# Performance work log

Hardware: AMD Instinct MI355X
Metric: run time of the kernel (lower is better)

## Reference

```python
import jax, jax.numpy as jnp
import numpy as np

NUM_HEADS = 8


def setup_inputs() -> dict:
    key = jax.random.key(0)
    ks = jax.random.split(key, 7)
    B, Tq, Tkv, J, C = 16, 243, 243, 17, 256
    q = jax.random.normal(ks[0], (B, Tq, J, C), dtype=jnp.float32)
    kv = jax.random.normal(ks[1], (B, Tkv, J, C), dtype=jnp.float32)
    s = 1.0 / np.sqrt(C)
    Wq = jax.random.normal(ks[2], (C, C), dtype=jnp.float32) * s
    Wk = jax.random.normal(ks[3], (C, C), dtype=jnp.float32) * s
    Wv = jax.random.normal(ks[4], (C, C), dtype=jnp.float32) * s
    Wp = jax.random.normal(ks[5], (C, C), dtype=jnp.float32) * s
    bp = jnp.zeros((C,), dtype=jnp.float32)
    return {"q": q, "kv": kv, "Wq": Wq, "Wk": Wk, "Wv": Wv, "Wp": Wp, "bp": bp}


def reference(q, kv, Wq, Wk, Wv, Wp, bp):
    # q: [B, Tq, J, C], kv: [B, Tkv, J, C]
    b, tq, j, d = q.shape
    t_kv = kv.shape[1]
    h = NUM_HEADS
    hd = d // h
    scale = hd ** (-0.5)

    def split_heads(x, t):
        # [B, T, J, C] -> [B, H, J, T, hd]  (matches permute(0,3,2,1,4))
        return x.reshape(b, t, j, h, hd).transpose(0, 3, 2, 1, 4)

    q_p = split_heads(q @ Wq.T, tq)
    k_p = split_heads(kv @ Wk.T, t_kv)
    v_p = split_heads(kv @ Wv.T, t_kv)

    # attn: [B, H, J, Tq, Tkv]
    attn = jnp.einsum('bhjqe,bhjke->bhjqk', q_p, k_p) * scale
    attn = jax.nn.softmax(attn, axis=-1)
    # out: [B, H, J, Tq, hd] -> [B, Tq, J, C]
    out = jnp.einsum('bhjqk,bhjke->bhjqe', attn, v_p)
    out = out.transpose(0, 3, 2, 1, 4).reshape(b, tq, j, d)
    out = out @ Wp.T + bp
    return (attn, out)
```

## Files before the change

kernel.cpp:

```cpp
#include <hip/hip_runtime.h>

typedef _Float16 f16;
typedef _Float16 f16x8 __attribute__((ext_vector_type(8)));
typedef _Float16 f16x4 __attribute__((ext_vector_type(4)));
typedef float f32x4 __attribute__((ext_vector_type(4)));
typedef float f32x4a __attribute__((ext_vector_type(4), aligned(4)));

#define B_DIM 16
#define T_DIM 243
#define J_DIM 17
#define C_DIM 256
#define H_DIM 8
#define HD_DIM 32
#define M_DIM (B_DIM * T_DIM * J_DIM)
#define NSLICE (B_DIM * H_DIM * J_DIM)
#define TJ (T_DIM * J_DIM)

#define QP_OFF 0ull
#define KP_OFF ((unsigned long long)NSLICE * T_DIM * HD_DIM)
#define VPT_OFF (2ull * KP_OFF)
#define O_OFF (VPT_OFF + (unsigned long long)NSLICE * HD_DIM * 256)
#define WF_OFF (O_OFF + (unsigned long long)M_DIM * C_DIM)
#define ATTN_SZ ((unsigned long long)NSLICE * T_DIM * T_DIM)

#define SWZ(row, col) ((col) ^ (((row) & 7) << 3))

__global__ __launch_bounds__(256)
void wconv_kernel(const float* __restrict__ Wq, const float* __restrict__ Wk,
                  const float* __restrict__ Wv, const float* __restrict__ Wp,
                  f16* __restrict__ wf)
{
    int i = blockIdx.x * 256 + threadIdx.x;
    const float* src = (i < 65536) ? Wq : (i < 131072) ? Wk : (i < 196608) ? Wv : Wp;
    wf[i] = (f16)src[i & 65535];
}

__global__ __launch_bounds__(256)
void proj_kernel(const float* __restrict__ q, const float* __restrict__ kv,
                 const f16* __restrict__ wf, f16* __restrict__ ws)
{
    const int which = blockIdx.z;
    const float* A = (which == 0) ? q : kv;
    const f16* W = wf + which * 65536;
    f16* out = ws + (which == 0 ? QP_OFF : KP_OFF);

    const int tid = threadIdx.x;
    const int w = tid >> 6, l = tid & 63;
    const int lm = l & 15, g = l >> 4;
    const int m0 = blockIdx.x * 64;

    int arow = m0 + w * 16 + lm;
    const bool mok = arow < M_DIM;
    if (!mok) arow = M_DIM - 1;
    const float* Ab = A + (size_t)arow * C_DIM + g * 8;

    f16x8 af[8];
#pragma unroll
    for (int kk = 0; kk < 8; ++kk) {
        f32x4 a0 = *(const f32x4*)(Ab + kk * 32);
        f32x4 a1 = *(const f32x4*)(Ab + kk * 32 + 4);
#pragma unroll
        for (int j = 0; j < 4; ++j) { af[kk][j] = (f16)a0[j]; af[kk][4 + j] = (f16)a1[j]; }
    }

    f32x4 acc[16] = {};
#pragma unroll
    for (int nt = 0; nt < 16; ++nt) {
        const f16* Wb = W + (size_t)(nt * 16 + lm) * C_DIM + g * 8;
#pragma unroll
        for (int kk = 0; kk < 8; ++kk) {
            f16x8 bf = *(const f16x8*)(Wb + kk * 32);
            acc[nt] = __builtin_amdgcn_mfma_f32_16x16x32_f16(bf, af[kk], acc[nt], 0, 0, 0);
        }
    }

    int b = arow / TJ;
    int rem = arow - b * TJ;
    int t = rem / J_DIM;
    int jj = rem - t * J_DIM;
    if (mok) {
#pragma unroll
        for (int nt = 0; nt < 16; ++nt) {
            int n0 = nt * 16 + g * 4;
            int h = n0 >> 5, e = n0 & 31;
            int sI = (b * H_DIM + h) * J_DIM + jj;
            f16x4 v;
#pragma unroll
            for (int r = 0; r < 4; ++r) v[r] = (f16)acc[nt][r];
            *(f16x4*)(out + (size_t)sI * (T_DIM * HD_DIM) + (size_t)t * HD_DIM + e) = v;
        }
    }
}

__global__ __launch_bounds__(256)
void vproj_kernel(const float* __restrict__ kv, const f16* __restrict__ wv,
                  f16* __restrict__ vpt)
{
    __shared__ f16 Sv[64 * 72];

    const int bj = blockIdx.z;
    const int b = bj / J_DIM, j = bj - b * J_DIM;
    const int t0 = blockIdx.x * 64;
    const int n0 = blockIdx.y * 64;

    const int tid = threadIdx.x;
    const int w = tid >> 6, l = tid & 63;
    const int lm = l & 15, g = l >> 4;

    int t = t0 + w * 16 + lm;
    if (t > T_DIM - 1) t = T_DIM - 1;
    const float* Ab = kv + ((size_t)b * TJ + (size_t)t * J_DIM + j) * C_DIM + g * 8;

    f16x8 af[8];
#pragma unroll
    for (int kk = 0; kk < 8; ++kk) {
        f32x4 a0 = *(const f32x4*)(Ab + kk * 32);
        f32x4 a1 = *(const f32x4*)(Ab + kk * 32 + 4);
#pragma unroll
        for (int jj = 0; jj < 4; ++jj) { af[kk][jj] = (f16)a0[jj]; af[kk][4 + jj] = (f16)a1[jj]; }
    }

    f32x4 acc[4] = {};
#pragma unroll
    for (int nt = 0; nt < 4; ++nt) {
        const f16* Wb = wv + (size_t)(n0 + nt * 16 + lm) * C_DIM + g * 8;
#pragma unroll
        for (int kk = 0; kk < 8; ++kk) {
            f16x8 bf = *(const f16x8*)(Wb + kk * 32);
            acc[nt] = __builtin_amdgcn_mfma_f32_16x16x32_f16(af[kk], bf, acc[nt], 0, 0, 0);
        }
    }

    const int trow = w * 16 + g * 4;
#pragma unroll
    for (int nt = 0; nt < 4; ++nt) {
        int nl = nt * 16 + lm;
#pragma unroll
        for (int r = 0; r < 4; ++r)
            Sv[nl * 72 + trow + r] = (f16)acc[nt][r];
    }
    __syncthreads();

    const int nl = tid >> 2, tp = tid & 3;
    const int n = n0 + nl;
    const int h = n >> 5, e = n & 31;
    const int s = (b * H_DIM + h) * J_DIM + j;
    const int tbase = t0 + tp * 16;

    f16x8 v0 = *(const f16x8*)&Sv[nl * 72 + tp * 16];
    f16x8 v1 = *(const f16x8*)&Sv[nl * 72 + tp * 16 + 8];
    if (tbase + 15 > T_DIM - 1) {
#pragma unroll
        for (int i = 0; i < 8; ++i) {
            if (tbase + i > T_DIM - 1) v0[i] = (f16)0;
            if (tbase + 8 + i > T_DIM - 1) v1[i] = (f16)0;
        }
    }
    f16* dst = vpt + (size_t)s * (HD_DIM * 256) + (size_t)e * 256 + tbase;
    *(f16x8*)dst = v0;
    *(f16x8*)(dst + 8) = v1;
}

__global__ __launch_bounds__(256)
void attn_kernel(const f16* __restrict__ ws_qp, const f16* __restrict__ ws_kp,
                 const f16* __restrict__ ws_vpt, f16* __restrict__ ws_o,
                 float* __restrict__ attn_out)
{
    __shared__ f16 S[64 * 256];

    const int s = blockIdx.y;
    const int q0 = blockIdx.x * 64;
    const int tid = threadIdx.x;
    const int w = tid >> 6, l = tid & 63;
    const int lm = l & 15, g = l >> 4;
    const float scale = 0.17677669529663687f;

    const f16* qpS = ws_qp + (size_t)s * (T_DIM * HD_DIM);
    const f16* kpS = ws_kp + (size_t)s * (T_DIM * HD_DIM);

    int qrow = q0 + w * 16 + lm;
    const bool qok = qrow < T_DIM;
    if (!qok) qrow = T_DIM - 1;
    f16x8 bq = *(const f16x8*)(qpS + qrow * HD_DIM + g * 8);

    float cv[16][4];
    f32x4 zero = {0.f, 0.f, 0.f, 0.f};
#pragma unroll
    for (int kt = 0; kt < 16; ++kt) {
        int krow = kt * 16 + lm;
        if (krow > T_DIM - 1) krow = T_DIM - 1;
        f16x8 ak = *(const f16x8*)(kpS + krow * HD_DIM + g * 8);
        f32x4 c = __builtin_amdgcn_mfma_f32_16x16x32_f16(ak, bq, zero, 0, 0, 0);
#pragma unroll
        for (int r = 0; r < 4; ++r) cv[kt][r] = c[r] * scale;
    }
#pragma unroll
    for (int r = 0; r < 4; ++r)
        if (g * 4 + r >= 3) cv[15][r] = -1e30f;

    float mx = -1e30f;
#pragma unroll
    for (int kt = 0; kt < 16; ++kt) {
        float a = fmaxf(fmaxf(cv[kt][0], cv[kt][1]), fmaxf(cv[kt][2], cv[kt][3]));
        mx = fmaxf(mx, a);
    }
    mx = fmaxf(mx, __shfl_xor(mx, 16));
    mx = fmaxf(mx, __shfl_xor(mx, 32));

    float s0 = 0.f, s1 = 0.f;
#pragma unroll
    for (int kt = 0; kt < 16; ++kt) {
        float p0 = __expf(cv[kt][0] - mx);
        float p1 = __expf(cv[kt][1] - mx);
        float p2 = __expf(cv[kt][2] - mx);
        float p3 = __expf(cv[kt][3] - mx);
        cv[kt][0] = p0; cv[kt][1] = p1; cv[kt][2] = p2; cv[kt][3] = p3;
        s0 += p0 + p1;
        s1 += p2 + p3;
    }
    float sum = s0 + s1;
    sum += __shfl_xor(sum, 16);
    sum += __shfl_xor(sum, 32);
    const float rinv = 1.0f / sum;

    float* drow = attn_out + (size_t)s * (T_DIM * T_DIM) + (size_t)qrow * T_DIM;
    const int qlocal = w * 16 + lm;
#pragma unroll
    for (int kt = 0; kt < 16; ++kt) {
        const int col0 = kt * 16 + g * 4;
        f16x4 pv4;
        f32x4a o4;
#pragma unroll
        for (int r = 0; r < 4; ++r) {
            float p = cv[kt][r] * rinv;
            o4[r] = p;
            pv4[r] = (f16)p;
        }
        *(f16x4*)&S[qlocal * 256 + SWZ(qlocal, col0)] = pv4;
        if (qok) {
            if (col0 + 3 < T_DIM) {
                *(f32x4a*)(drow + col0) = o4;
            } else if (col0 < T_DIM) {
                drow[col0] = o4[0];
                drow[col0 + 1] = o4[1];
                drow[col0 + 2] = o4[2];
            }
        }
    }
    __syncthreads();

    const f16* vpS = ws_vpt + (size_t)s * (HD_DIM * 256);
    f32x4 o0 = {}, o1 = {};
    const int prow = w * 16 + lm;
#pragma unroll
    for (int kk = 0; kk < 8; ++kk) {
        f16x8 ap = *(const f16x8*)(&S[prow * 256 + SWZ(prow, kk * 32 + g * 8)]);
        f16x8 b0 = *(const f16x8*)(vpS + (size_t)(0 * 16 + lm) * 256 + kk * 32 + g * 8);
        f16x8 b1 = *(const f16x8*)(vpS + (size_t)(1 * 16 + lm) * 256 + kk * 32 + g * 8);
        o0 = __builtin_amdgcn_mfma_f32_16x16x32_f16(ap, b0, o0, 0, 0, 0);
        o1 = __builtin_amdgcn_mfma_f32_16x16x32_f16(ap, b1, o1, 0, 0, 0);
    }

    int b = s / (H_DIM * J_DIM);
    int rem = s - b * (H_DIM * J_DIM);
    int h = rem / J_DIM;
    int jj = rem - h * J_DIM;
#pragma unroll
    for (int r = 0; r < 4; ++r) {
        int qr = q0 + w * 16 + g * 4 + r;
        if (qr >= T_DIM) continue;
        size_t m = (size_t)b * TJ + (size_t)qr * J_DIM + jj;
        ws_o[m * 256 + h * 32 + lm] = (f16)o0[r];
        ws_o[m * 256 + h * 32 + 16 + lm] = (f16)o1[r];
    }
}

__global__ __launch_bounds__(256)
void outproj_kernel(const f16* __restrict__ ws_o, const f16* __restrict__ wpf,
                    const float* __restrict__ bp, float* __restrict__ out)
{
    const int tid = threadIdx.x;
    const int w = tid >> 6, l = tid & 63;
    const int lm = l & 15, g = l >> 4;
    const int m0 = blockIdx.x * 64;

    int m = m0 + w * 16 + lm;
    const bool mok = m < M_DIM;
    if (!mok) m = M_DIM - 1;
    const f16* Ab = ws_o + (size_t)m * C_DIM + g * 8;
    f16x8 af[8];
#pragma unroll
    for (int kk = 0; kk < 8; ++kk) af[kk] = *(const f16x8*)(Ab + kk * 32);

    f32x4 acc[16] = {};
#pragma unroll
    for (int nt = 0; nt < 16; ++nt) {
        const f16* Wb = wpf + (size_t)(nt * 16 + lm) * C_DIM + g * 8;
#pragma unroll
        for (int kk = 0; kk < 8; ++kk) {
            f16x8 bf = *(const f16x8*)(Wb + kk * 32);
            acc[nt] = __builtin_amdgcn_mfma_f32_16x16x32_f16(bf, af[kk], acc[nt], 0, 0, 0);
        }
    }

    if (mok) {
#pragma unroll
        for (int nt = 0; nt < 16; ++nt) {
            int n0 = nt * 16 + g * 4;
            f32x4a bv = *(const f32x4a*)(bp + n0);
            f32x4a o;
#pragma unroll
            for (int r = 0; r < 4; ++r) o[r] = acc[nt][r] + bv[r];
            *(f32x4a*)(out + (size_t)m * C_DIM + n0) = o;
        }
    }
}

extern "C" void kernel_launch(void* const* d_in, const int* in_sizes, int n_in,
                              void* d_out, int out_size, void* d_ws, size_t ws_size,
                              hipStream_t stream)
{
    const float* q  = (const float*)d_in[0];
    const float* kv = (const float*)d_in[1];
    const float* Wq = (const float*)d_in[2];
    const float* Wk = (const float*)d_in[3];
    const float* Wv = (const float*)d_in[4];
    const float* Wp = (const float*)d_in[5];
    const float* bp = (const float*)d_in[6];
    float* attn_out = (float*)d_out;
    float* out = attn_out + ATTN_SZ;
    f16* ws = (f16*)d_ws;

    wconv_kernel<<<dim3(1024), dim3(256), 0, stream>>>(Wq, Wk, Wv, Wp, ws + WF_OFF);

    dim3 gp((M_DIM + 63) / 64, 1, 2);
    proj_kernel<<<gp, dim3(256), 0, stream>>>(q, kv, ws + WF_OFF, ws);

    dim3 gv(4, 4, B_DIM * J_DIM);
    vproj_kernel<<<gv, dim3(256), 0, stream>>>(kv, ws + WF_OFF + 2 * 65536, ws + VPT_OFF);

    dim3 ga(4, NSLICE);
    attn_kernel<<<ga, dim3(256), 0, stream>>>(ws + QP_OFF, ws + KP_OFF, ws + VPT_OFF,
                                              ws + O_OFF, attn_out);

    dim3 go((M_DIM + 63) / 64, 1);
    outproj_kernel<<<go, dim3(256), 0, stream>>>(ws + O_OFF, ws + WF_OFF + 3 * 65536, bp, out);
}
```

Baseline: 598.7 us.

## Stage K tile in LDS, fold softmax scale into Q projection, coalesce attn writes

The softmax scale is folded into the Q projection epilogue, so the attention kernel no longer multiplies every score. Each block now copies the per-slice K tile into rotated (swizzled) shared memory once and reads K fragments from LDS rather than global memory. The fp32 attention matrix is written row-contiguously from the f16 probabilities held in shared memory, giving coalesced stores. The stored attention values are now rounded through f16, which lowers their precision, and two extra barriers are added.

```diff
diff --git a/kernel.cpp b/kernel.cpp
--- a/kernel.cpp
+++ b/kernel.cpp
@@ -43,6 +43,7 @@
     const float* A = (which == 0) ? q : kv;
     const f16* W = wf + which * 65536;
     f16* out = ws + (which == 0 ? QP_OFF : KP_OFF);
+    const float osc = (which == 0) ? 0.17677669529663687f : 1.0f;
 
     const int tid = threadIdx.x;
     const int w = tid >> 6, l = tid & 63;
@@ -86,7 +87,7 @@
             int sI = (b * H_DIM + h) * J_DIM + jj;
             f16x4 v;
 #pragma unroll
-            for (int r = 0; r < 4; ++r) v[r] = (f16)acc[nt][r];
+            for (int r = 0; r < 4; ++r) v[r] = (f16)(acc[nt][r] * osc);
             *(f16x4*)(out + (size_t)sI * (T_DIM * HD_DIM) + (size_t)t * HD_DIM + e) = v;
         }
     }
@@ -173,26 +174,48 @@
     const int tid = threadIdx.x;
     const int w = tid >> 6, l = tid & 63;
     const int lm = l & 15, g = l >> 4;
-    const float scale = 0.17677669529663687f;
 
     const f16* qpS = ws_qp + (size_t)s * (T_DIM * HD_DIM);
     const f16* kpS = ws_kp + (size_t)s * (T_DIM * HD_DIM);
 
+    {
+        const int t = tid;
+        char* drow = (char*)S + t * 64;
+        const int rot = t >> 3;
+        if (t < T_DIM) {
+            const f16* src = kpS + t * HD_DIM;
+#pragma unroll
+            for (int gp = 0; gp < 4; ++gp) {
+                f16x8 v = *(const f16x8*)(src + gp * 8);
+                *(f16x8*)(drow + 16 * ((gp + rot) & 3)) = v;
+            }
+        } else {
+            f16x8 z = {};
+#pragma unroll
+            for (int gp = 0; gp < 4; ++gp)
+                *(f16x8*)(drow + 16 * ((gp + rot) & 3)) = z;
+        }
+    }
+
     int qrow = q0 + w * 16 + lm;
-    const bool qok = qrow < T_DIM;
-    if (!qok) qrow = T_DIM - 1;
+    const bool qok_load = qrow < T_DIM;
+    if (!qok_load) qrow = T_DIM - 1;
     f16x8 bq = *(const f16x8*)(qpS + qrow * HD_DIM + g * 8);
 
+    __syncthreads();
+
+    const char* kb = (const char*)S + lm * 64;
+    const int rb = g + (lm >> 3);
+    const int off_e = 16 * (rb & 3);
+    const int off_o = 16 * ((rb + 2) & 3);
     float cv[16][4];
     f32x4 zero = {0.f, 0.f, 0.f, 0.f};
 #pragma unroll
     for (int kt = 0; kt < 16; ++kt) {
-        int krow = kt * 16 + lm;
-        if (krow > T_DIM - 1) krow = T_DIM - 1;
-        f16x8 ak = *(const f16x8*)(kpS + krow * HD_DIM + g * 8);
+        f16x8 ak = *(const f16x8*)(kb + kt * 1024 + ((kt & 1) ? off_o : off_e));
         f32x4 c = __builtin_amdgcn_mfma_f32_16x16x32_f16(ak, bq, zero, 0, 0, 0);
 #pragma unroll
-        for (int r = 0; r < 4; ++r) cv[kt][r] = c[r] * scale;
+        for (int r = 0; r < 4; ++r) cv[kt][r] = c[r];
     }
 #pragma unroll
     for (int r = 0; r < 4; ++r)
@@ -223,31 +246,37 @@
     sum += __shfl_xor(sum, 32);
     const float rinv = 1.0f / sum;
 
-    float* drow = attn_out + (size_t)s * (T_DIM * T_DIM) + (size_t)qrow * T_DIM;
+    __syncthreads();
+
     const int qlocal = w * 16 + lm;
 #pragma unroll
     for (int kt = 0; kt < 16; ++kt) {
         const int col0 = kt * 16 + g * 4;
         f16x4 pv4;
-        f32x4a o4;
-#pragma unroll
-        for (int r = 0; r < 4; ++r) {
-            float p = cv[kt][r] * rinv;
-            o4[r] = p;
-            pv4[r] = (f16)p;
-        }
+#pragma unroll
+        for (int r = 0; r < 4; ++r) pv4[r] = (f16)(cv[kt][r] * rinv);
         *(f16x4*)&S[qlocal * 256 + SWZ(qlocal, col0)] = pv4;
-        if (qok) {
-            if (col0 + 3 < T_DIM) {
-                *(f32x4a*)(drow + col0) = o4;
-            } else if (col0 < T_DIM) {
-                drow[col0] = o4[0];
-                drow[col0 + 1] = o4[1];
-                drow[col0 + 2] = o4[2];
+    }
+
+    float* dst = attn_out + (size_t)s * (T_DIM * T_DIM);
+#pragma unroll
+    for (int rr = 0; rr < 16; ++rr) {
+        const int row = w * 16 + rr;
+        const int qr = q0 + row;
+        if (qr < T_DIM) {
+            const int col = l * 4;
+            f16x4 pv = *(const f16x4*)&S[row * 256 + SWZ(row, col)];
+            float* p = dst + (size_t)qr * T_DIM + col;
+            if (col + 3 < T_DIM) {
+                f32x4a o4;
+#pragma unroll
+                for (int r = 0; r < 4; ++r) o4[r] = (float)pv[r];
+                *(f32x4a*)p = o4;
+            } else if (col < T_DIM) {
+                p[0] = (float)pv[0]; p[1] = (float)pv[1]; p[2] = (float)pv[2];
             }
         }
     }
-    __syncthreads();
 
     const f16* vpS = ws_vpt + (size_t)s * (HD_DIM * 256);
     f32x4 o0 = {}, o1 = {};
```

After: 551.6 us. -7.9%, faster.
